# Optimization experiments

Hardware: AMD Instinct MI355X
Metric: run time of the kernel (lower is better)

The kernel has to match this reference:

```python
import jax, jax.numpy as jnp
import numpy as np

TOP_K = 15
TEMPERATURE = 1.0
NEG_SLOPE = 0.2


def setup_inputs() -> dict:
    key = jax.random.key(0)
    ks = jax.random.split(key, 6)
    N, H, heads, hd = 4096, 256, 4, 64
    E_c = 131072
    embeddings = jax.random.normal(ks[0], (N, H), dtype=jnp.float32)
    # nn.Linear(H, heads*hd, bias=False) weight: [heads*hd, H], xavier-ish scale
    W = jax.random.normal(ks[1], (heads * hd, H), dtype=jnp.float32) * (1.0 / np.sqrt(H))
    att = jax.random.normal(ks[2], (heads, 2 * hd), dtype=jnp.float32) * 0.1
    corr_lambda = jnp.ones((1,), dtype=jnp.float32)
    sector_mask = jax.random.uniform(ks[3], (N, N)) > 0.05
    active_mask = jnp.ones((N,), dtype=bool)
    corr_edge_index = jax.random.randint(ks[4], (2, E_c), 0, N)
    corr_edge_weight = jax.random.uniform(ks[5], (E_c,), minval=-1.0, maxval=1.0)
    return dict(embeddings=embeddings, W=W, att=att, corr_lambda=corr_lambda,
                sector_mask=sector_mask, active_mask=active_mask,
                corr_edge_index=corr_edge_index, corr_edge_weight=corr_edge_weight)


def reference(embeddings, W, att, corr_lambda, sector_mask, active_mask,
              corr_edge_index, corr_edge_weight):
    N = embeddings.shape[0]
    heads = att.shape[0]
    hd = att.shape[1] // 2
    # h: [N, heads, hd]
    h = (embeddings @ W.T).reshape(N, heads, hd)
    # algebraic split of concat([h_i || h_j]) . att  ->  s_dst[i] + s_src[j]
    a_dst, a_src = att[:, :hd], att[:, hd:]
    s_dst = jnp.einsum('nhd,hd->nh', h, a_dst)  # coefficient of row node i
    s_src = jnp.einsum('nhd,hd->nh', h, a_src)  # coefficient of col node j
    # [N, N, heads] broadcast-add, leaky_relu, mean over heads
    scores = jax.nn.leaky_relu(s_dst[:, None, :] + s_src[None, :, :], NEG_SLOPE)
    scores = scores.mean(axis=-1) / TEMPERATURE  # [N, N]
    mask = (active_mask[:, None] & active_mask[None, :]) & sector_mask  # [N, N]
    scores = jnp.where(mask, scores, -jnp.inf)
    # correlation prior scattered into a dense matrix (index-assign semantics)
    corr = jnp.zeros((N, N), dtype=scores.dtype).at[
        corr_edge_index[0], corr_edge_index[1]].set(corr_edge_weight.astype(scores.dtype))
    corr = corr * mask.astype(scores.dtype)
    scores = scores + corr_lambda[0] * corr
    k = min(TOP_K, N - 1)
    topk_scores, topk_idx = jax.lax.top_k(scores, k)  # per-row top-k over src dim
    rows = jnp.broadcast_to(jnp.arange(N)[:, None], (N, k))
    # dense mask guarantees all top-k entries are finite -> E = N*k fixed
    edge_index = jnp.stack([topk_idx.reshape(-1), rows.reshape(-1)], axis=0)  # [2, N*k]
    edge_weight = jax.nn.softmax(topk_scores, axis=1).reshape(-1)  # [N*k]
    return edge_index, edge_weight
```

## Files before the change

kernel.cpp:

```cpp
#include <hip/hip_runtime.h>
#include <math.h>

#define H_DIM 256
#define HEADS 4
#define HD 64
#define TOPK 15
#define NSLOPE 0.2
#define NSLOPEF 0.2f
#define EDGE_CAP_MAX 128
#define CAND_CAP 256
#define SROWS 16

__global__ __launch_bounds__(256) void prep1_kernel(const float* __restrict__ W,
                                                    const float* __restrict__ att,
                                                    double* __restrict__ wa_dst,
                                                    double* __restrict__ wa_src,
                                                    int* __restrict__ cnt,
                                                    unsigned int* __restrict__ abits,
                                                    const int* __restrict__ active) {
    const int b = blockIdx.x;
    cnt[b * 256 + threadIdx.x] = 0;
    if (b < 2 * HEADS) {
        const int k = threadIdx.x;
        const int h = b >> 1;
        const int side = b & 1;
        double a = 0.0;
        for (int d = 0; d < HD; ++d)
            a += (double)W[(h * HD + d) * H_DIM + k] * (double)att[h * 2 * HD + side * HD + d];
        (side ? wa_src : wa_dst)[h * H_DIM + k] = a;
    } else if (b == 8 && threadIdx.x < 128) {
        const int* ap = active + threadIdx.x * 32;
        unsigned int wv = 0;
        for (int t = 0; t < 32; ++t)
            if (ap[t]) wv |= 1u << t;
        abits[threadIdx.x] = wv;
    }
}

__global__ __launch_bounds__(256) void prep2_kernel(
    const float* __restrict__ emb, const double* __restrict__ wa_dst,
    const double* __restrict__ wa_src, double* __restrict__ s_dst,
    double* __restrict__ s_src, float* __restrict__ s_dst_f,
    float* __restrict__ s_src_f, const int* __restrict__ eidx,
    const float* __restrict__ ew, int* __restrict__ cnt,
    int4* __restrict__ etab, int N, int E, int cap, int sblocks) {
    const int b = blockIdx.x;
    const int tid = threadIdx.x;

    if (b < sblocks) {
        __shared__ double wa_l[8][258];
        __shared__ float emb_l[SROWS][258];
        const int i0 = b * SROWS;
#pragma unroll
        for (int c = 0; c < 8; ++c)
            wa_l[c][tid] = ((c & 1) ? wa_src : wa_dst)[(c >> 1) * H_DIM + tid];
#pragma unroll
        for (int r = 0; r < SROWS; ++r)
            emb_l[r][tid] = emb[(size_t)(i0 + r) * H_DIM + tid];
        __syncthreads();

        const int j = tid >> 1;
        const int half = tid & 1;
        const int r = j >> 3;
        const int c = j & 7;
        const int base = half * 128;
        double acc = 0.0;
#pragma unroll 8
        for (int k = 0; k < 128; ++k)
            acc += (double)emb_l[r][base + k] * wa_l[c][base + k];
        const double other = __shfl_xor(acc, 1, 64);
        const double lo = half ? other : acc;
        const double hi = half ? acc : other;
        const double s = lo + hi;
        if (half == 0) {
            const int i = i0 + r;
            const int h = c >> 1;
            if (c & 1) {
                s_src[i * HEADS + h] = s;
                s_src_f[i * HEADS + h] = (float)s;
            } else {
                s_dst[i * HEADS + h] = s;
                s_dst_f[i * HEADS + h] = (float)s;
            }
        }
    } else {
        const int e = (b - sblocks) * 256 + tid;
        if (e < E) {
            const int r = eidx[e];
            const int cc = eidx[E + e];
            const int s = atomicAdd(&cnt[r], 1);
            if (s < cap) {
                int4 rec;
                rec.x = cc;
                rec.y = e;
                rec.z = __float_as_int(ew[e]);
                rec.w = 0;
                etab[r * cap + s] = rec;
            }
        }
    }
}

#define FOR16(OP) OP(0) OP(1) OP(2) OP(3) OP(4) OP(5) OP(6) OP(7) \
                  OP(8) OP(9) OP(10) OP(11) OP(12) OP(13) OP(14) OP(15)

__global__ __launch_bounds__(256) void main_kernel(
    const double* __restrict__ s_dst, const double* __restrict__ s_src,
    const float* __restrict__ s_dst_f, const float* __restrict__ s_src_f,
    const int* __restrict__ sector_mask, const unsigned short* __restrict__ abits16,
    const int* __restrict__ active, const float* __restrict__ lam_p,
    const int* __restrict__ cnt, const int4* __restrict__ etab,
    float* __restrict__ out, int N, int cap) {
    const int i = blockIdx.x;
    const int tid = threadIdx.x;
    const int lane = tid & 63;
    const int wid = tid >> 6;

    __shared__ int ec[EDGE_CAP_MAX];
    __shared__ int ee[EDGE_CAP_MAX];
    __shared__ float ewl[EDGE_CAP_MAX];
    __shared__ int wcol[EDGE_CAP_MAX];
    __shared__ double wadd[EDGE_CAP_MAX];
    __shared__ unsigned int wth[4];
    __shared__ double cand_v[CAND_CAP];
    __shared__ int cand_i[CAND_CAP];
    __shared__ int cand_cnt, wcnt;
    __shared__ double sorted_v[TOPK];
    __shared__ int sorted_i[TOPK];
    __shared__ double exps[TOPK];

    if (tid == 0) { cand_cnt = 0; wcnt = 0; }

    int deg = cnt[i];
    if (deg > cap) deg = cap;
    for (int p = tid; p < deg; p += 256) {
        const int4 rec = etab[i * cap + p];
        ec[p] = rec.x;
        ee[p] = rec.y;
        ewl[p] = __int_as_float(rec.z);
    }
    __syncthreads();

    const int* mrow = sector_mask + (size_t)i * N;
    const int4 m0 = *(const int4*)(mrow + 16 * tid);
    const int4 m1 = *(const int4*)(mrow + 16 * tid + 4);
    const int4 m2 = *(const int4*)(mrow + 16 * tid + 8);
    const int4 m3 = *(const int4*)(mrow + 16 * tid + 12);
    const unsigned int act_us = (unsigned int)abits16[tid];
    unsigned int pb = 0;
#define PB(C, VAL) if ((VAL) != 0) pb |= (1u << (C));
    PB(0, m0.x)  PB(1, m0.y)  PB(2, m0.z)  PB(3, m0.w)
    PB(4, m1.x)  PB(5, m1.y)  PB(6, m1.z)  PB(7, m1.w)
    PB(8, m2.x)  PB(9, m2.y)  PB(10, m2.z) PB(11, m2.w)
    PB(12, m3.x) PB(13, m3.y) PB(14, m3.z) PB(15, m3.w)
#undef PB
    pb &= act_us;

    const int lhi = lane >> 4;
    const int llo = lane & 15;
    unsigned int pm = 0;
#pragma unroll
    for (int k = 0; k < 16; ++k) {
        const unsigned int opb = (unsigned int)__shfl((int)pb, 4 * k + lhi, 64);
        pm |= ((opb >> llo) & 1u) << k;
    }
    if (active[i] == 0) pm = 0;

    const float sdf0 = s_dst_f[i * 4 + 0];
    const float sdf1 = s_dst_f[i * 4 + 1];
    const float sdf2 = s_dst_f[i * 4 + 2];
    const float sdf3 = s_dst_f[i * 4 + 3];
    const double sd0 = s_dst[i * 4 + 0];
    const double sd1 = s_dst[i * 4 + 1];
    const double sd2 = s_dst[i * 4 + 2];
    const double sd3 = s_dst[i * 4 + 3];
    const double lam = (double)lam_p[0];
    const double4* __restrict__ s_src4 = (const double4*)s_src;
    const float4* __restrict__ s_srcf4 = (const float4*)s_src_f;
    const int jbase = (wid << 10) | lane;

    float f0, f1, f2, f3, f4, f5, f6, f7, f8, f9, f10, f11, f12, f13, f14, f15;
#define INIT_SLOT(K) { \
    const bool m = (pm >> K) & 1u; \
    const float4 sv = s_srcf4[jbase + (K << 6)]; \
    float x0 = sdf0 + sv.x, x1 = sdf1 + sv.y, x2 = sdf2 + sv.z, x3 = sdf3 + sv.w; \
    x0 = (x0 < 0.0f) ? NSLOPEF * x0 : x0; \
    x1 = (x1 < 0.0f) ? NSLOPEF * x1 : x1; \
    x2 = (x2 < 0.0f) ? NSLOPEF * x2 : x2; \
    x3 = (x3 < 0.0f) ? NSLOPEF * x3 : x3; \
    f##K = m ? (0.25f * (x0 + x1 + x2 + x3)) : -INFINITY; }
    FOR16(INIT_SLOT)
#undef INIT_SLOT

    if (tid < deg) {
        const int c = ec[tid];
        const int eid = ee[tid];
        bool win = true;
        for (int q = 0; q < deg; ++q)
            if (ec[q] == c && ee[q] > eid) win = false;
        if (win) {
            int p = atomicAdd(&wcnt, 1);
            wcol[p] = c;
            wadd[p] = lam * (double)ewl[tid];
        }
    }
    __syncthreads();

    const int nw = wcnt;
    for (int w = 0; w < nw; ++w) {
        const int c = wcol[w];
        if ((((c >> 10) << 6) | (c & 63)) == tid) {
            const float addf = (float)wadd[w];
            const int kk = (c >> 6) & 15;
#define ADD_SLOT(K) if (kk == K) f##K += addf;
            FOR16(ADD_SLOT)
#undef ADD_SLOT
        }
    }

    unsigned int k0, k1, k2, k3, k4, k5, k6, k7, k8, k9, k10, k11, k12, k13, k14, k15;
#define KEY_SLOT(K) { const unsigned u = __float_as_uint(f##K); \
    k##K = u ^ ((unsigned)((int)u >> 31) | 0x80000000u); }
    FOR16(KEY_SLOT)
#undef KEY_SLOT
    unsigned int lmax = k0;
#define LMAX(K) if (k##K > lmax) lmax = k##K;
    FOR16(LMAX)
#undef LMAX

    unsigned int th = 0;
    for (int b = 31; b >= 0; --b) {
        const unsigned int trial = th | (1u << b);
        unsigned long long m = __ballot(lmax >= trial);
        if (__popcll(m) >= TOPK) th = trial;
    }
    if (lane == 0) wth[wid] = th;
    __syncthreads();
    th = wth[0];
    if (wth[1] > th) th = wth[1];
    if (wth[2] > th) th = wth[2];
    if (wth[3] > th) th = wth[3];
    th = (th > 256u) ? (th - 256u) : 0u;

#define FILT(K) if (k##K >= th) { int p = atomicAdd(&cand_cnt, 1); \
    if (p < CAND_CAP) cand_i[p] = jbase + (K << 6); }
    FOR16(FILT)
#undef FILT
    __syncthreads();

    int C = cand_cnt;
    if (C > CAND_CAP) C = CAND_CAP;
    if (tid < C) {
        const int j = cand_i[tid];
        const double4 sv = s_src4[j];
        double x0 = sd0 + sv.x, x1 = sd1 + sv.y, x2 = sd2 + sv.z, x3 = sd3 + sv.w;
        x0 = (x0 < 0.0) ? NSLOPE * x0 : x0;
        x1 = (x1 < 0.0) ? NSLOPE * x1 : x1;
        x2 = (x2 < 0.0) ? NSLOPE * x2 : x2;
        x3 = (x3 < 0.0) ? NSLOPE * x3 : x3;
        double v = 0.25 * (x0 + x1 + x2 + x3);
        for (int w = 0; w < nw; ++w)
            if (wcol[w] == j) v += wadd[w];
        cand_v[tid] = v;
    }
    __syncthreads();

    if (tid < C) {
        const double mv = cand_v[tid];
        const int mi = cand_i[tid];
        int rank = 0;
        for (int q = 0; q < C; ++q) {
            const double qv = cand_v[q];
            const int qi = cand_i[q];
            rank += ((qv > mv) || (qv == mv && qi < mi)) ? 1 : 0;
        }
        if (rank < TOPK) { sorted_v[rank] = mv; sorted_i[rank] = mi; }
    }
    __syncthreads();

    if (tid < TOPK) exps[tid] = exp(sorted_v[tid] - sorted_v[0]);
    __syncthreads();
    if (tid < TOPK) {
        double s = 0.0;
        for (int t = 0; t < TOPK; ++t) s += exps[t];
        const int NK = N * TOPK;
        const int base = i * TOPK + tid;
        out[base] = (float)sorted_i[tid];
        out[NK + base] = (float)i;
        out[2 * NK + base] = (float)(exps[tid] / s);
    }
}

extern "C" void kernel_launch(void* const* d_in, const int* in_sizes, int n_in,
                              void* d_out, int out_size, void* d_ws, size_t ws_size,
                              hipStream_t stream) {
    const float* emb    = (const float*)d_in[0];
    const float* W      = (const float*)d_in[1];
    const float* att    = (const float*)d_in[2];
    const float* lam    = (const float*)d_in[3];
    const int*   sector = (const int*)d_in[4];
    const int*   active = (const int*)d_in[5];
    const int*   eidx   = (const int*)d_in[6];
    const float* ew     = (const float*)d_in[7];
    float* out = (float*)d_out;

    const int N = in_sizes[5];
    const int E = in_sizes[6] / 2;

    double* wa_dst = (double*)d_ws;
    double* wa_src = wa_dst + HEADS * H_DIM;
    double* s_dst  = wa_src + HEADS * H_DIM;
    double* s_src  = s_dst + (size_t)N * HEADS;
    float* s_dst_f = (float*)(s_src + (size_t)N * HEADS);
    float* s_src_f = s_dst_f + (size_t)N * HEADS;
    int* cnt       = (int*)(s_src_f + (size_t)N * HEADS);
    unsigned int* abits = (unsigned int*)(cnt + N);
    uintptr_t ep = (uintptr_t)(abits + N / 32);
    ep = (ep + 15) & ~(uintptr_t)15;
    int4* etab = (int4*)ep;

    size_t used = (ep - (uintptr_t)d_ws) + 64;
    size_t rem = (ws_size > used) ? (ws_size - used) : 0;
    int cap = (int)(rem / ((size_t)N * 16));
    if (cap > EDGE_CAP_MAX) cap = EDGE_CAP_MAX;
    if (cap < 16) cap = 16;

    const int nb = (E + 255) / 256;
    const int sblocks = N / SROWS;

    prep1_kernel<<<16, 256, 0, stream>>>(W, att, wa_dst, wa_src, cnt, abits, active);
    prep2_kernel<<<sblocks + nb, 256, 0, stream>>>(emb, wa_dst, wa_src, s_dst, s_src,
                                                   s_dst_f, s_src_f, eidx, ew, cnt,
                                                   etab, N, E, cap, sblocks);
    main_kernel<<<N, 256, 0, stream>>>(s_dst, s_src, s_dst_f, s_src_f, sector,
                                       (const unsigned short*)abits, active, lam, cnt,
                                       etab, out, N, cap);
}
```

Before: 177.9 us.

## Fuse prep kernels, scatter correlation adds via shared table, shorten threshold search

Merges the two prep kernels into one, so each score block recomputes W·att projections itself and the count array is zeroed with a memset instead of a separate kernel. In the main kernel, winning correlation edges write into a dense 4096-entry shared-memory table, and every thread gathers its 16 slots from it instead of looping over all winner edges with compare chains. The ballot threshold search skips the low 8 bits. This removes a launch and a serial per-edge loop, at the cost of 16KB more LDS per block (possibly lower occupancy) and redundant W·att work in every prep block.

Result: slower. 185.2 us (+4.1%).

```diff
diff --git a/kernel.cpp b/kernel.cpp
--- a/kernel.cpp
+++ b/kernel.cpp
@@ -11,39 +11,15 @@
 #define CAND_CAP 256
 #define SROWS 16
 
-__global__ __launch_bounds__(256) void prep1_kernel(const float* __restrict__ W,
-                                                    const float* __restrict__ att,
-                                                    double* __restrict__ wa_dst,
-                                                    double* __restrict__ wa_src,
-                                                    int* __restrict__ cnt,
-                                                    unsigned int* __restrict__ abits,
-                                                    const int* __restrict__ active) {
-    const int b = blockIdx.x;
-    cnt[b * 256 + threadIdx.x] = 0;
-    if (b < 2 * HEADS) {
-        const int k = threadIdx.x;
-        const int h = b >> 1;
-        const int side = b & 1;
-        double a = 0.0;
-        for (int d = 0; d < HD; ++d)
-            a += (double)W[(h * HD + d) * H_DIM + k] * (double)att[h * 2 * HD + side * HD + d];
-        (side ? wa_src : wa_dst)[h * H_DIM + k] = a;
-    } else if (b == 8 && threadIdx.x < 128) {
-        const int* ap = active + threadIdx.x * 32;
-        unsigned int wv = 0;
-        for (int t = 0; t < 32; ++t)
-            if (ap[t]) wv |= 1u << t;
-        abits[threadIdx.x] = wv;
-    }
-}
-
-__global__ __launch_bounds__(256) void prep2_kernel(
-    const float* __restrict__ emb, const double* __restrict__ wa_dst,
-    const double* __restrict__ wa_src, double* __restrict__ s_dst,
-    double* __restrict__ s_src, float* __restrict__ s_dst_f,
-    float* __restrict__ s_src_f, const int* __restrict__ eidx,
-    const float* __restrict__ ew, int* __restrict__ cnt,
-    int4* __restrict__ etab, int N, int E, int cap, int sblocks) {
+__global__ __launch_bounds__(256) void prep_kernel(
+    const float* __restrict__ W, const float* __restrict__ att,
+    const float* __restrict__ emb,
+    double* __restrict__ s_dst, double* __restrict__ s_src,
+    float* __restrict__ s_dst_f, float* __restrict__ s_src_f,
+    const int* __restrict__ eidx, const float* __restrict__ ew,
+    int* __restrict__ cnt, int4* __restrict__ etab,
+    const int* __restrict__ active, unsigned int* __restrict__ abits,
+    int N, int E, int cap, int sblocks) {
     const int b = blockIdx.x;
     const int tid = threadIdx.x;
 
@@ -51,9 +27,20 @@
         __shared__ double wa_l[8][258];
         __shared__ float emb_l[SROWS][258];
         const int i0 = b * SROWS;
-#pragma unroll
-        for (int c = 0; c < 8; ++c)
-            wa_l[c][tid] = ((c & 1) ? wa_src : wa_dst)[(c >> 1) * H_DIM + tid];
+
+        {
+            double a[8] = {0, 0, 0, 0, 0, 0, 0, 0};
+            for (int d = 0; d < HD; ++d) {
+#pragma unroll
+                for (int h = 0; h < HEADS; ++h) {
+                    const double wv = (double)W[(h * HD + d) * H_DIM + tid];
+                    a[2 * h] += wv * (double)att[h * 2 * HD + d];
+                    a[2 * h + 1] += wv * (double)att[h * 2 * HD + HD + d];
+                }
+            }
+#pragma unroll
+            for (int c = 0; c < 8; ++c) wa_l[c][tid] = a[c];
+        }
 #pragma unroll
         for (int r = 0; r < SROWS; ++r)
             emb_l[r][tid] = emb[(size_t)(i0 + r) * H_DIM + tid];
@@ -84,6 +71,13 @@
             }
         }
     } else {
+        if (b == sblocks && tid < 128) {
+            const int* ap = active + tid * 32;
+            unsigned int wv = 0;
+            for (int t = 0; t < 32; ++t)
+                if (ap[t]) wv |= 1u << t;
+            abits[tid] = wv;
+        }
         const int e = (b - sblocks) * 256 + tid;
         if (e < E) {
             const int r = eidx[e];
@@ -121,6 +115,7 @@
     __shared__ float ewl[EDGE_CAP_MAX];
     __shared__ int wcol[EDGE_CAP_MAX];
     __shared__ double wadd[EDGE_CAP_MAX];
+    __shared__ float addf_l[4096];
     __shared__ unsigned int wth[4];
     __shared__ double cand_v[CAND_CAP];
     __shared__ int cand_i[CAND_CAP];
@@ -130,6 +125,13 @@
     __shared__ double exps[TOPK];
 
     if (tid == 0) { cand_cnt = 0; wcnt = 0; }
+
+    {
+        const float4 z = make_float4(0.f, 0.f, 0.f, 0.f);
+        float4* a4 = (float4*)addf_l;
+#pragma unroll
+        for (int z4 = 0; z4 < 4; ++z4) a4[tid + (z4 << 8)] = z;
+    }
 
     int deg = cnt[i];
     if (deg > cap) deg = cap;
@@ -199,24 +201,19 @@
         for (int q = 0; q < deg; ++q)
             if (ec[q] == c && ee[q] > eid) win = false;
         if (win) {
+            const double a = lam * (double)ewl[tid];
             int p = atomicAdd(&wcnt, 1);
             wcol[p] = c;
-            wadd[p] = lam * (double)ewl[tid];
+            wadd[p] = a;
+            addf_l[c] = (float)a;
         }
     }
     __syncthreads();
 
     const int nw = wcnt;
-    for (int w = 0; w < nw; ++w) {
-        const int c = wcol[w];
-        if ((((c >> 10) << 6) | (c & 63)) == tid) {
-            const float addf = (float)wadd[w];
-            const int kk = (c >> 6) & 15;
-#define ADD_SLOT(K) if (kk == K) f##K += addf;
-            FOR16(ADD_SLOT)
-#undef ADD_SLOT
-        }
-    }
+#define ADDG(K) f##K += addf_l[jbase + (K << 6)];
+    FOR16(ADDG)
+#undef ADDG
 
     unsigned int k0, k1, k2, k3, k4, k5, k6, k7, k8, k9, k10, k11, k12, k13, k14, k15;
 #define KEY_SLOT(K) { const unsigned u = __float_as_uint(f##K); \
@@ -229,7 +226,7 @@
 #undef LMAX
 
     unsigned int th = 0;
-    for (int b = 31; b >= 0; --b) {
+    for (int b = 31; b >= 8; --b) {
         const unsigned int trial = th | (1u << b);
         unsigned long long m = __ballot(lmax >= trial);
         if (__popcll(m) >= TOPK) th = trial;
@@ -307,9 +304,7 @@
     const int N = in_sizes[5];
     const int E = in_sizes[6] / 2;
 
-    double* wa_dst = (double*)d_ws;
-    double* wa_src = wa_dst + HEADS * H_DIM;
-    double* s_dst  = wa_src + HEADS * H_DIM;
+    double* s_dst  = (double*)d_ws;
     double* s_src  = s_dst + (size_t)N * HEADS;
     float* s_dst_f = (float*)(s_src + (size_t)N * HEADS);
     float* s_src_f = s_dst_f + (size_t)N * HEADS;
@@ -328,10 +323,11 @@
     const int nb = (E + 255) / 256;
     const int sblocks = N / SROWS;
 
-    prep1_kernel<<<16, 256, 0, stream>>>(W, att, wa_dst, wa_src, cnt, abits, active);
-    prep2_kernel<<<sblocks + nb, 256, 0, stream>>>(emb, wa_dst, wa_src, s_dst, s_src,
-                                                   s_dst_f, s_src_f, eidx, ew, cnt,
-                                                   etab, N, E, cap, sblocks);
+    hipMemsetAsync(cnt, 0, (size_t)N * sizeof(int), stream);
+    prep_kernel<<<sblocks + nb, 256, 0, stream>>>(W, att, emb, s_dst, s_src,
+                                                  s_dst_f, s_src_f, eidx, ew, cnt,
+                                                  etab, active, abits, N, E, cap,
+                                                  sblocks);
     main_kernel<<<N, 256, 0, stream>>>(s_dst, s_src, s_dst_f, s_src_f, sector,
                                        (const unsigned short*)abits, active, lam, cnt,
                                        etab, out, N, cap);
```
